# Performance work log

Hardware: AMD Instinct MI355X
Metric: run time of the kernel (lower is better)

## Reference

```python
import jax, jax.numpy as jnp
import numpy as np

N_EVENTS = 50000
TS_SIZE = 512
N_NEURONS = 256
LAMBDA_HOMEO = 0.25


def setup_inputs() -> dict:
    key = jax.random.key(0)
    k1, k2 = jax.random.split(key)
    # event time surfaces (nonnegative, like torch surfaces)
    all_ts = jax.random.uniform(k1, (N_EVENTS, TS_SIZE), dtype=jnp.float32)
    # synapses.weight ~ U[0,1), as in torch.nn.init.uniform_(a=0,b=1)
    W = jax.random.uniform(k2, (N_NEURONS, TS_SIZE), dtype=jnp.float32)
    cumhisto = jnp.ones((N_NEURONS,), dtype=jnp.float32)
    return {"all_ts": all_ts, "W": W, "cumhisto": cumhisto}


def reference(all_ts, W, cumhisto):
    """Training branch (learning_flag=True, homeo_flag=True) of hotslayer.forward.

    Sequential per-event: normalize ts, cosine-like scores beta, homeostatic gain
    picks the winner, winner row of W is pulled toward ts, histogram incremented.
    Returns (per-event winners [N_EVENTS], final W [N,TS], final cumhisto [N]).
    """
    n_neurons = W.shape[0]

    def step(carry, ts):
        W, ch = carry
        ts = ts / jnp.linalg.norm(ts)
        w_norm = jnp.linalg.norm(W, axis=1)          # [N]
        beta = (W @ ts) / w_norm                      # [N]
        gain = jnp.exp(LAMBDA_HOMEO * (1.0 - n_neurons * ch / ch.sum()))
        n_star = jnp.argmax(gain * beta)
        Ck = W[n_star]                                # [TS]
        alpha = 0.01 / (1.0 + ch[n_star] / 20000.0)
        W = W.at[n_star].set(Ck + alpha * beta[n_star] * (ts - Ck))
        ch = ch.at[n_star].add(1.0)
        return (W, ch), n_star

    (W_f, ch_f), winners = jax.lax.scan(step, (W, cumhisto), all_ts)
    return winners, W_f, ch_f
```

## Files before the change

### kernel.cpp

```cpp
#include <hip/hip_runtime.h>
#include <hip/hip_bf16.h>

#define N_EVENTS 50000
#define TS 512
#define NN 256
#define BATCH 512
#define SUB 64
#define LAMB 0.25f
#define NB 98

#define RLF(v, l) __int_as_float(__builtin_amdgcn_readlane(__float_as_int(v), (l)))
#define RLI(v, l) __builtin_amdgcn_readlane((v), (l))
#define FRCP(x) __builtin_amdgcn_rcpf(x)
#define FRSQ(x) __builtin_amdgcn_rsqf(x)
#define DPP_MAXF(x, ctrl)                                                            \
    { int _s = __builtin_amdgcn_update_dpp(__float_as_int(x), __float_as_int(x),     \
                                           (ctrl), 0xF, 0xF, false);                 \
      (x) = fmaxf((x), __int_as_float(_s)); }


__global__ __launch_bounds__(256)
void inv_kernel(const float* __restrict__ ts, float* __restrict__ inv)
{
    __shared__ double red[256];
    const int e = blockIdx.x;
    const int d = threadIdx.x;
    const float* row = ts + (size_t)e * TS;
    float x0 = row[d], x1 = row[d + 256];
    red[d] = (double)x0 * x0 + (double)x1 * x1;
    __syncthreads();
    for (int st = 128; st > 0; st >>= 1) {
        if (d < st) red[d] += red[d + st];
        __syncthreads();
    }
    if (d == 0) inv[e] = (float)(1.0 / sqrt(red[0]));
}

__global__ __launch_bounds__(256)
void init_kernel(const float* __restrict__ chin, float* __restrict__ ch,
                 float* Pn0, float* Pn1, float* phi0, float* phi1,
                 float* c0, float* c1, float* d0, float* d1,
                 int* w0, int* w1)
{
    int i = blockIdx.x * 256 + threadIdx.x;
    if (i < NN) { ch[i] = chin[i]; Pn0[i] = 1.f; Pn1[i] = 1.f; }
    if (i < BATCH) {
        phi0[i] = 0.f; phi1[i] = 0.f; c0[i] = 0.f; c1[i] = 0.f;
        d0[i] = 0.f; d1[i] = 0.f; w0[i] = 0; w1[i] = 0;
    }
}


__device__ void gram_tile(float* SH, const float* __restrict__ ts,
                          const float* __restrict__ inv,
                          int astart, int as, int bstart2, int bs2,
                          int be, int bf, float* __restrict__ outp, int transpose)
{
    float* At = SH;
    float* Bt = SH + 64 * 33;
    if (be * 64 >= as || bf * 64 >= bs2) return;
    const int tx = threadIdx.x & 15, ty = threadIdx.x >> 4;
    float acc[4][4] = {};
    for (int kt = 0; kt < TS; kt += 32) {
        for (int it = threadIdx.x; it < 64 * 32; it += 256) {
            int r = it >> 5, c = it & 31;
            int ra = be * 64 + r, rb = bf * 64 + r;
            At[r * 33 + c] = (ra < as) ? ts[(size_t)(astart + ra) * TS + kt + c] : 0.f;
            Bt[r * 33 + c] = (rb < bs2) ? ts[(size_t)(bstart2 + rb) * TS + kt + c] : 0.f;
        }
        __syncthreads();
#pragma unroll
        for (int kk = 0; kk < 32; ++kk) {
            float av[4], bv[4];
#pragma unroll
            for (int i = 0; i < 4; ++i) av[i] = At[(ty * 4 + i) * 33 + kk];
#pragma unroll
            for (int j = 0; j < 4; ++j) bv[j] = Bt[(tx * 4 + j) * 33 + kk];
#pragma unroll
            for (int i = 0; i < 4; ++i)
#pragma unroll
                for (int j = 0; j < 4; ++j)
                    acc[i][j] += av[i] * bv[j];
        }
        __syncthreads();
    }
#pragma unroll
    for (int i = 0; i < 4; ++i) {
        int e = be * 64 + ty * 4 + i;
        if (e >= as) continue;
        float ie = inv[astart + e];
#pragma unroll
        for (int j = 0; j < 4; ++j) {
            int f = bf * 64 + tx * 4 + j;
            if (f >= bs2) continue;
            float v = acc[i][j] * ie * inv[bstart2 + f];
            if (transpose) outp[(size_t)f * BATCH + e] = v;
            else           outp[(size_t)e * BATCH + f] = v;
        }
    }
}

__global__ __launch_bounds__(256)
void gram_kernel(const float* __restrict__ ts, const float* __restrict__ inv,
                 float* __restrict__ outp, int astart, int as, int bstart2, int bs2,
                 int upper, int transpose)
{
    __shared__ float SHg[64 * 33 * 2];
    if (upper && (int)blockIdx.y < (int)blockIdx.x) return;
    gram_tile(SHg, ts, inv, astart, as, bstart2, bs2, blockIdx.x, blockIdx.y,
              outp, transpose);
}


__device__ void neuron_body(float* shf, double* red,
    const float* __restrict__ ts, const float* __restrict__ inv,
    const float* __restrict__ Wsrc, float* __restrict__ wdst,
    const int* __restrict__ winPrev, const float* __restrict__ phiPrev,
    const float* __restrict__ PnPrev,
    float* __restrict__ wn2W, float* __restrict__ S2W,
    const float* __restrict__ chbuf, float* __restrict__ chout,
    int n, int bprev_start, int bs_prev, int bnext_start, int bs_next)
{
    int* winS = (int*)shf;
    float* phiS = shf + 512;
    float* WL = shf + 1024;
    const int d = threadIdx.x;
    for (int i = d; i < bs_prev; i += 256) { winS[i] = winPrev[i]; phiS[i] = phiPrev[i]; }
    __syncthreads();
    const float Pf = PnPrev[n];
    float w0 = Wsrc[n * TS + d];
    float w1 = Wsrc[n * TS + d + 256];
    double a0 = 0.0, a1 = 0.0;
    for (int e = 0; e < bs_prev; ++e) {
        if (winS[e] == n) {
            double coef = (double)phiS[e];
            float iv = inv[bprev_start + e];
            const float* tr = ts + (size_t)(bprev_start + e) * TS;
            a0 += coef * (double)(tr[d] * iv);
            a1 += coef * (double)(tr[d + 256] * iv);
        }
    }
    w0 = (float)((double)Pf * ((double)w0 + a0));
    w1 = (float)((double)Pf * ((double)w1 + a1));
    wdst[n * TS + d] = w0;
    wdst[n * TS + d + 256] = w1;
    WL[d] = w0; WL[d + 256] = w1;
    if (wn2W) {
        red[d] = (double)w0 * w0 + (double)w1 * w1;
        __syncthreads();
        for (int st = 128; st > 0; st >>= 1) {
            if (d < st) red[d] += red[d + st];
            __syncthreads();
        }
        if (d == 0) wn2W[n] = (float)red[0];
    } else {
        __syncthreads();
    }
    if (bs_next > 0) {
#pragma unroll
        for (int rep = 0; rep < 2; ++rep) {
            int f = d + rep * 256;
            if (f < bs_next) {
                double acc = 0.0;
                const float* tr = ts + (size_t)(bnext_start + f) * TS;
                for (int k = 0; k < TS; ++k) acc += (double)tr[k] * (double)WL[k];
                S2W[f * NN + n] = (float)(acc * (double)inv[bnext_start + f]);
            }
        }
    }
    if (chout && d == 0) chout[n] = chbuf[n];
}

__global__ __launch_bounds__(256)
void neuron_kernel(const float* __restrict__ ts, const float* __restrict__ inv,
    const float* __restrict__ Wsrc, float* __restrict__ wdst,
    const int* __restrict__ winPrev, const float* __restrict__ phiPrev,
    const float* __restrict__ PnPrev,
    float* __restrict__ wn2W, float* __restrict__ S2W,
    const float* __restrict__ chbuf, float* __restrict__ chout,
    int bprev_start, int bs_prev, int bnext_start, int bs_next)
{
    __shared__ float SHN[1536];
    __shared__ double redN[256];
    neuron_body(SHN, redN, ts, inv, Wsrc, wdst, winPrev, phiPrev, PnPrev,
                wn2W, S2W, chbuf, chout, blockIdx.x,
                bprev_start, bs_prev, bnext_start, bs_next);
}


__global__ __launch_bounds__(256)
void fix_kernel(const float* __restrict__ S2r, const float* __restrict__ GxTr,
    const int* __restrict__ winPrev, const float* __restrict__ phiPrev,
    const float* __restrict__ cPrev, const float* __restrict__ dPrev,
    const float* __restrict__ PnPrev, const float* __restrict__ wn2b,
    float* __restrict__ S0corr, float* __restrict__ wn2start,
    int bs, int b0flag)
{
    __shared__ int winS[512];
    __shared__ float phiP[512];
    __shared__ float gr[512];
    __shared__ float cS[512];
    __shared__ float dS[512];
    const int tid = threadIdx.x;
    const int f = blockIdx.x;
    for (int i = tid; i < 512; i += 256) {
        int w = winPrev[i];
        winS[i] = w;
        phiP[i] = b0flag ? 0.f : phiPrev[i] * PnPrev[w];
        cS[i] = cPrev[i];
        dS[i] = dPrev[i];
        gr[i] = (b0flag || f >= bs) ? 0.f : GxTr[(size_t)f * BATCH + i];
    }
    __syncthreads();
    if (f < bs) {
        int n = tid;
        float acc = PnPrev[n] * S2r[f * NN + n];
        if (!b0flag) {
            for (int e = 0; e < 512; ++e)
                if (winS[e] == n) acc += phiP[e] * gr[e];
        }
        S0corr[f * NN + n] = acc;
    }
    if (f == 0 && tid < 64) {
        const int lane = tid;
        float w2[4];
#pragma unroll
        for (int k = 0; k < 4; ++k) w2[k] = wn2b[k * 64 + lane];
        for (int e = 0; e < 512; ++e) {
            float c = cS[e];
            if (c != 0.f) {
                int w = winS[e];
                int owner = w & 63, kk = w >> 6;
                float omc = 1.f - c;
                float t2 = 2.f * c * omc * dS[e] + c * c;
#pragma unroll
                for (int k = 0; k < 4; ++k)
                    if (lane == owner && k == kk) w2[k] = omc * omc * w2[k] + t2;
            }
        }
#pragma unroll
        for (int k = 0; k < 4; ++k) wn2start[k * 64 + lane] = w2[k];
    }
}


__device__ void block0_body(float* SH,
    const float* __restrict__ S0corr, const float* __restrict__ GwR,
    const float* __restrict__ wn2start, float* __restrict__ chbuf,
    int* __restrict__ winCur, float* __restrict__ phiCur,
    float* __restrict__ cCur, float* __restrict__ dotCur, float* __restrict__ PnCur,
    float* __restrict__ winners_out, int bstart, int bs)
{
    float* ACC = SH;
    float* GS  = SH + 16384;
    float* GL  = SH + 20480;
    int*   winL = (int*)(SH + 24576);
    float* phiL = SH + 25088;
    float* cL   = SH + 25600;
    float* dL   = SH + 26112;
    unsigned long long* CANDu = (unsigned long long*)(SH + 26624);
    float* SUMS = SH + 26640;

    const int tid = threadIdx.x, wid = tid >> 6, lane = tid & 63;
    const int widu = __builtin_amdgcn_readfirstlane(wid);
    const int myn = (wid << 6) + lane;

    const float KC = -(LAMB * 256.0f * 1.44269504f);
    float ch = chbuf[myn];
    float wn2v = wn2start[myn];
    float rn = FRSQ(wn2v);
    float al = 0.01f * FRCP(1.0f + ch * (1.0f / 20000.0f));
    float Pn = 1.0f;

    {
        float loc = ch;
#pragma unroll
        for (int off = 32; off > 0; off >>= 1) loc += __shfl_xor(loc, off, 64);
        if (lane == 0) SUMS[wid] = loc;
    }
    __syncthreads();
    const float Sbase = SUMS[0] + SUMS[1] + SUMS[2] + SUMS[3];

    const int nsub = (bs + SUB - 1) >> 6;
    for (int sub = 0; sub < nsub; ++sub) {
        const int s0 = sub << 6;
        const int cnt = min(SUB, bs - s0);
        __syncthreads();
        {
            const int n = tid;
            for (int f = 0; f < cnt; f += 8) {
                const float* src = S0corr + (size_t)(s0 + f) * NN + n;
                float v0 = src[0 * NN], v1 = src[1 * NN], v2 = src[2 * NN], v3 = src[3 * NN];
                float v4 = src[4 * NN], v5 = src[5 * NN], v6 = src[6 * NN], v7 = src[7 * NN];
                ACC[(f + 0) * NN + ((n + f + 0) & 255)] = v0;
                ACC[(f + 1) * NN + ((n + f + 1) & 255)] = v1;
                ACC[(f + 2) * NN + ((n + f + 2) & 255)] = v2;
                ACC[(f + 3) * NN + ((n + f + 3) & 255)] = v3;
                ACC[(f + 4) * NN + ((n + f + 4) & 255)] = v4;
                ACC[(f + 5) * NN + ((n + f + 5) & 255)] = v5;
                ACC[(f + 6) * NN + ((n + f + 6) & 255)] = v6;
                ACC[(f + 7) * NN + ((n + f + 7) & 255)] = v7;
            }
        }
        for (int it = tid; it < SUB * SUB; it += 256) {
            int t = it >> 6, f = it & 63;
            GS[it] = (t < cnt && f < cnt) ? GwR[(size_t)(s0 + t) * BATCH + s0 + f] : 0.f;
        }
        for (int base = 0; base < s0; base += 64) {
            {
                const int i0 = tid, i1 = tid + 256, i2 = tid + 512, i3 = tid + 768;
                for (int rep = 0; rep < 4096; rep += 1024) {
                    float g0 = GwR[(size_t)(base + ((i0 + rep) >> 6)) * BATCH + s0 + (i0 & 63)];
                    float g1 = GwR[(size_t)(base + ((i1 + rep) >> 6)) * BATCH + s0 + (i1 & 63)];
                    float g2 = GwR[(size_t)(base + ((i2 + rep) >> 6)) * BATCH + s0 + (i2 & 63)];
                    float g3 = GwR[(size_t)(base + ((i3 + rep) >> 6)) * BATCH + s0 + (i3 & 63)];
                    GL[i0 + rep] = g0; GL[i1 + rep] = g1;
                    GL[i2 + rep] = g2; GL[i3 + rep] = g3;
                }
            }
            int wreg = winL[base + lane];
            float preg = phiL[base + lane];
            __syncthreads();
            for (int j = 0; j < 64; ++j) {
                int wj = RLI(wreg, j);
                if ((wj & 3) == wid) {
                    float pj = RLF(preg, j);
                    if (lane < cnt)
                        ACC[lane * NN + ((wj + lane) & 255)] += pj * GL[j * 64 + lane];
                }
            }
            __syncthreads();
        }
        __syncthreads();

        float acur = ACC[myn & 255];
        for (int t = 0; t < cnt; ++t) {
            const int ib = s0 + t;
            const float K2 = KC * FRCP(Sbase + (float)ib);
            const bool havenext = (t + 1 < cnt);
            float anext = 0.f;
            if (havenext) anext = ACC[(t + 1) * NN + ((myn + t + 1) & 255)];
            const int forig = t + 1 + lane;
            const float gval = GS[t * SUB + (forig & 63)];

            const float pa = Pn * acur;
            const float beta = pa * rn;
            const float key = beta * exp2f(K2 * ch);
            float kmax = key;
            DPP_MAXF(kmax, 0x111); DPP_MAXF(kmax, 0x112); DPP_MAXF(kmax, 0x114);
            DPP_MAXF(kmax, 0x118); DPP_MAXF(kmax, 0x142); DPP_MAXF(kmax, 0x143);
            const float smax = RLF(kmax, 63);
            unsigned long long mm = __ballot(key == smax);
            if (lane == 0) {
                int nl = (int)__builtin_ctzll(mm);
                CANDu[((t & 1) << 2) + wid] =
                    ((unsigned long long)__float_as_uint(smax) << 32)
                    | (unsigned)(255 - ((wid << 6) + nl));
            }
            __syncthreads();
            const unsigned long long* cb = CANDu + ((t & 1) << 2);
            unsigned long long b0 = cb[0], b1 = cb[1], b2 = cb[2], b3 = cb[3];
            unsigned long long ba = b0 > b1 ? b0 : b1;
            unsigned long long bb = b2 > b3 ? b2 : b3;
            unsigned long long best = ba > bb ? ba : bb;
            int ns = 255 - (int)(best & 0xFFull);
            ns = __builtin_amdgcn_readfirstlane(ns);
            const int ksq = ns >> 6, owner = ns & 63;

            if (widu == ksq) {
                const float betas  = RLF(beta, owner);
                const float dots   = RLF(pa, owner);
                const float pold   = RLF(Pn, owner);
                const float alphas = RLF(al, owner);
                const float c    = alphas * betas;
                const float omc  = 1.0f - c;
                const float pnew = pold * omc;
                const float phi  = c * FRCP(pnew);
                const float g1   = RLF(gval, 0);
                if (lane == owner) {
                    wn2v = omc * omc * wn2v + 2.f * c * omc * dots + c * c;
                    rn = FRSQ(wn2v);
                    ch += 1.0f;
                    al = 0.01f * FRCP(1.0f + ch * (1.0f / 20000.0f));
                    Pn = pnew;
                    if (havenext) anext += phi * g1;
                }
                if (lane > 0 && forig < cnt)
                    ACC[forig * NN + ((ns + forig) & 255)] += phi * gval;
                if (lane == 0) {
                    winL[ib] = ns; phiL[ib] = phi;
                    cL[ib] = c; dL[ib] = dots;
                }
            }
            acur = anext;
        }
    }
    __syncthreads();
    chbuf[myn] = ch;
    PnCur[myn] = Pn;
    for (int i = tid; i < bs; i += 256) {
        int w = winL[i];
        winCur[i] = w;
        phiCur[i] = phiL[i];
        cCur[i] = cL[i];
        dotCur[i] = dL[i];
        winners_out[bstart + i] = (float)w;
    }
}


__global__ __launch_bounds__(256)
void fusedA_kernel(const float* __restrict__ ts, const float* __restrict__ inv,
    const float* __restrict__ S0corr, const float* __restrict__ GwR,
    float* __restrict__ GwW, float* __restrict__ GxTW,
    const float* __restrict__ wn2start, float* __restrict__ chbuf,
    const int* __restrict__ winPrev, const float* __restrict__ phiPrev,
    const float* __restrict__ PnPrev,
    int* __restrict__ winCur, float* __restrict__ phiCur,
    float* __restrict__ cCur, float* __restrict__ dotCur, float* __restrict__ PnCur,
    float* __restrict__ Wcur, float* __restrict__ wn2W, float* __restrict__ S2W,
    float* __restrict__ out, int b, int bstart, int bs, int bnext_start, int bs_next)
{
    __shared__ float SH[26656];
    const int bx = blockIdx.x;
    if (bx == 0) {
        block0_body(SH, S0corr, GwR, wn2start, chbuf,
                    winCur, phiCur, cCur, dotCur, PnCur, out, bstart, bs);
    } else if (bx <= NN) {
        neuron_body(SH, (double*)(SH + 1536), ts, inv, Wcur, Wcur,
                    winPrev, phiPrev, PnPrev, wn2W, S2W, nullptr, nullptr,
                    bx - 1, bstart - BATCH, (b == 0) ? 0 : BATCH,
                    bnext_start, bs_next);
    } else {
        int job = bx - (NN + 1);
        if (bs_next <= 0) return;
        if (job < 64) {
            gram_tile(SH, ts, inv, bstart, bs, bnext_start, bs_next,
                      job >> 3, job & 7, GxTW, 1);
        } else {
            int jw = job - 64;
            int be = 0;
            while (jw >= 8 - be) { jw -= 8 - be; ++be; }
            int bf = be + jw;
            gram_tile(SH, ts, inv, bnext_start, bs_next, bnext_start, bs_next,
                      be, bf, GwW, 0);
        }
    }
}


__global__ __launch_bounds__(256)
void winit_kernel(const float* __restrict__ Wcur, const float* __restrict__ chin,
                  float* __restrict__ ch, float* __restrict__ wn2, float* __restrict__ rn)
{
    __shared__ double red[256];
    const int n = blockIdx.x;
    const int d = threadIdx.x;
    float w0 = Wcur[n * TS + d], w1 = Wcur[n * TS + d + 256];
    red[d] = (double)w0 * w0 + (double)w1 * w1;
    __syncthreads();
    for (int st = 128; st > 0; st >>= 1) {
        if (d < st) red[d] += red[d + st];
        __syncthreads();
    }
    if (d == 0) {
        double s = red[0];
        wn2[n] = (float)s;
        rn[n]  = (float)(1.0 / sqrt(s));
        ch[n]  = chin[n];
    }
}

__global__ __launch_bounds__(256)
void s0_gemm_kernel(const float* __restrict__ ts, const float* __restrict__ Wcur,
                    const float* __restrict__ inv, float* __restrict__ S0P,
                    int bstart, int bs)
{
    __shared__ float At[64][33];
    __shared__ float Bt[64][33];
    const int bf = blockIdx.x;
    const int bn = blockIdx.y;
    if (bf * 64 >= bs) return;
    const int tx = threadIdx.x & 15, ty = threadIdx.x >> 4;
    double acc[4][4] = {};
    for (int kt = 0; kt < TS; kt += 32) {
        for (int it = threadIdx.x; it < 64 * 32; it += 256) {
            int r = it >> 5, c = it & 31;
            int row = bf * 64 + r;
            At[r][c] = (row < bs) ? ts[(size_t)(bstart + row) * TS + kt + c] : 0.f;
            Bt[r][c] = Wcur[(bn * 64 + r) * TS + kt + c];
        }
        __syncthreads();
#pragma unroll
        for (int kk = 0; kk < 32; ++kk) {
            float av[4], bv[4];
#pragma unroll
            for (int i = 0; i < 4; ++i) av[i] = At[ty * 4 + i][kk];
#pragma unroll
            for (int j = 0; j < 4; ++j) bv[j] = Bt[tx * 4 + j][kk];
#pragma unroll
            for (int i = 0; i < 4; ++i)
#pragma unroll
                for (int j = 0; j < 4; ++j)
                    acc[i][j] += (double)av[i] * (double)bv[j];
        }
        __syncthreads();
    }
#pragma unroll
    for (int i = 0; i < 4; ++i) {
        int f = bf * 64 + ty * 4 + i;
        if (f >= bs) continue;
        double iv = (double)inv[bstart + f];
#pragma unroll
        for (int j = 0; j < 4; ++j) {
            int n = bn * 64 + tx * 4 + j;
            S0P[f * NN + n] = (float)(acc[i][j] * iv);
        }
    }
}

__global__ __launch_bounds__(256)
void seq_step_kernel(const float* __restrict__ S0P, const float* __restrict__ Gb,
                     float* __restrict__ ch_g, const float* __restrict__ wn2_g,
                     const float* __restrict__ rn_g, float* __restrict__ Pn_g,
                     float* __restrict__ phi_g, int* __restrict__ win_g,
                     float* __restrict__ winners_out, int bstart, int bs)
{
    __shared__ float ACC[SUB * NN];
    __shared__ float GS[SUB * SUB];
    __shared__ float GL[SUB * SUB];
    __shared__ int   winL[BATCH];
    __shared__ float phiL[BATCH];

    const int tid = threadIdx.x;
    const int wid = tid >> 6;
    const int lane = tid & 63;

    float ch[4] = {0, 0, 0, 0}, wn2v[4] = {1, 1, 1, 1};
    float rn[4] = {1, 1, 1, 1}, Pn[4] = {1, 1, 1, 1};
    float Ssum = 1.f, sinv = 1.f;
    if (wid == 0) {
#pragma unroll
        for (int k = 0; k < 4; ++k) {
            int n = k * 64 + lane;
            ch[k]   = ch_g[n];
            wn2v[k] = wn2_g[n];
            rn[k]   = rn_g[n];
            Pn[k]   = 1.0f;
        }
        float loc = ch[0] + ch[1] + ch[2] + ch[3];
#pragma unroll
        for (int off = 32; off > 0; off >>= 1) loc += __shfl_xor(loc, off, 64);
        Ssum = loc;
        sinv = 1.0f / Ssum;
    }

    const int nsub = (bs + SUB - 1) >> 6;
    for (int sub = 0; sub < nsub; ++sub) {
        const int s0 = sub << 6;
        const int cnt = min(SUB, bs - s0);
        __syncthreads();

        for (int it = tid; it < cnt * NN; it += 256) {
            int r = it >> 8, n = it & 255;
            ACC[r * NN + ((n + r) & 255)] = S0P[(s0 + r) * NN + n];
        }
        for (int it = tid; it < cnt * SUB; it += 256) {
            int t = it >> 6, f = it & 63;
            GS[t * SUB + f] = (f < cnt) ? Gb[(s0 + t) * BATCH + s0 + f] : 0.f;
        }
        __syncthreads();

        for (int base = 0; base < s0; base += 64) {
            for (int it = tid; it < 64 * 64; it += 256)
                GL[it] = Gb[(base + (it >> 6)) * BATCH + s0 + (it & 63)];
            int   wreg = winL[base + lane];
            float preg = phiL[base + lane];
            __syncthreads();
            for (int j = 0; j < 64; ++j) {
                int wj = RLI(wreg, j);
                if ((wj & 3) == wid) {
                    float pj = RLF(preg, j);
                    if (lane < cnt)
                        ACC[lane * NN + ((wj + lane) & 255)] += pj * GL[j * 64 + lane];
                }
            }
            __syncthreads();
        }

        if (wid == 0) {
            float acur[4];
#pragma unroll
            for (int k = 0; k < 4; ++k) acur[k] = ACC[(k * 64 + lane) & 255];

            for (int t = 0; t < cnt; ++t) {
                const bool havenext = (t + 1 < cnt);
                float anext[4] = {0.f, 0.f, 0.f, 0.f};
                if (havenext) {
                    const int r = t + 1;
#pragma unroll
                    for (int k = 0; k < 4; ++k)
                        anext[k] = ACC[r * NN + ((k * 64 + lane + r) & 255)];
                }
                const int forig = t + 1 + lane;
                const float gval = GS[t * SUB + (forig & 63)];

                const float gmul = 256.0f * sinv;
                float beta[4], key[4];
                float kmax;
#pragma unroll
                for (int k = 0; k < 4; ++k) {
                    float dot = Pn[k] * acur[k];
                    beta[k] = dot * rn[k];
                    float frac = ch[k] * gmul;
                    float gain = __expf(LAMB * (1.0f - frac));
                    key[k] = gain * beta[k];
                }
                kmax = fmaxf(fmaxf(key[0], key[1]), fmaxf(key[2], key[3]));
                DPP_MAXF(kmax, 0x111); DPP_MAXF(kmax, 0x112); DPP_MAXF(kmax, 0x114);
                DPP_MAXF(kmax, 0x118); DPP_MAXF(kmax, 0x142); DPP_MAXF(kmax, 0x143);
                const float smax = RLF(kmax, 63);

                unsigned long long m0 = __ballot(key[0] == smax);
                unsigned long long m1 = __ballot(key[1] == smax);
                unsigned long long m2 = __ballot(key[2] == smax);
                unsigned long long m3 = __ballot(key[3] == smax);
                int ns = m0 ? (int)__builtin_ctzll(m0)
                       : m1 ? 64  + (int)__builtin_ctzll(m1)
                       : m2 ? 128 + (int)__builtin_ctzll(m2)
                            : 192 + (int)__builtin_ctzll(m3);
                ns = __builtin_amdgcn_readfirstlane(ns);
                const int owner = ns & 63, ks = ns >> 6;

                float bsel = (ks == 0) ? beta[0] : (ks == 1) ? beta[1] : (ks == 2) ? beta[2] : beta[3];
                float csel = (ks == 0) ? ch[0]   : (ks == 1) ? ch[1]   : (ks == 2) ? ch[2]   : ch[3];
                float asel = (ks == 0) ? acur[0] : (ks == 1) ? acur[1] : (ks == 2) ? acur[2] : acur[3];
                float psel = (ks == 0) ? Pn[0]   : (ks == 1) ? Pn[1]   : (ks == 2) ? Pn[2]   : Pn[3];
                const float betas = RLF(bsel, owner);
                const float chs   = RLF(csel, owner);
                const float dots  = RLF(psel * asel, owner);
                const float pold  = RLF(psel, owner);

                const float alpha = 0.01f / (1.0f + chs / 20000.0f);
                const float c    = alpha * betas;
                const float omc  = 1.0f - c;
                const float pnew = pold * omc;
                const float phi  = c / pnew;
                const float g1   = RLF(gval, 0);

#pragma unroll
                for (int k = 0; k < 4; ++k) {
                    bool me = (lane == owner) && (k == ks);
                    if (me) {
                        wn2v[k] = omc * omc * wn2v[k] + 2.f * c * omc * dots + c * c;
                        rn[k] = 1.0f / sqrtf(wn2v[k]);
                        ch[k] += 1.0f;
                        Pn[k] = pnew;
                        anext[k] += phi * g1;
                    }
                }
                if (lane > 0 && forig < cnt)
                    ACC[forig * NN + ((ns + forig) & 255)] += phi * gval;

                const int ib = s0 + t;
                if (lane == 0) {
                    winL[ib] = ns; phiL[ib] = phi;
                    win_g[ib] = ns; phi_g[ib] = phi;
                    winners_out[bstart + ib] = (float)ns;
                }
                Ssum += 1.0f;
                sinv = 1.0f / Ssum;
                if (havenext) {
#pragma unroll
                    for (int k = 0; k < 4; ++k) acur[k] = anext[k];
                }
            }
        }
        __syncthreads();
    }

    if (wid == 0) {
#pragma unroll
        for (int k = 0; k < 4; ++k) {
            int n = k * 64 + lane;
            ch_g[n] = ch[k];
            Pn_g[n] = Pn[k];
        }
    }
}

__global__ __launch_bounds__(256)
void wupdate_kernel(const float* __restrict__ ts, const float* __restrict__ inv,
                    const int* __restrict__ win_g, const float* __restrict__ phi_g,
                    const float* __restrict__ Pn_g, float* __restrict__ Wcur,
                    float* __restrict__ wn2_g, float* __restrict__ rn_g,
                    int bstart, int bs)
{
    __shared__ int   winS[BATCH];
    __shared__ float phiS[BATCH];
    __shared__ double red[256];
    const int n = blockIdx.x;
    const int d = threadIdx.x;
    for (int i = d; i < bs; i += 256) { winS[i] = win_g[i]; phiS[i] = phi_g[i]; }
    __syncthreads();
    const float Pf = Pn_g[n];
    float w0 = Wcur[n * TS + d];
    float w1 = Wcur[n * TS + d + 256];
    double a0 = 0.0, a1 = 0.0;
    for (int ib = 0; ib < bs; ++ib) {
        if (winS[ib] == n) {
            double coef = (double)phiS[ib] * (double)Pf;
            float iv = inv[bstart + ib];
            const float* tr = ts + (size_t)(bstart + ib) * TS;
            a0 += coef * (double)(tr[d] * iv);
            a1 += coef * (double)(tr[d + 256] * iv);
        }
    }
    w0 = (float)((double)Pf * (double)w0 + a0);
    w1 = (float)((double)Pf * (double)w1 + a1);
    Wcur[n * TS + d] = w0;
    Wcur[n * TS + d + 256] = w1;
    red[d] = (double)w0 * w0 + (double)w1 * w1;
    __syncthreads();
    for (int st = 128; st > 0; st >>= 1) {
        if (d < st) red[d] += red[d + st];
        __syncthreads();
    }
    if (d == 0) {
        double s = red[0];
        wn2_g[n] = (float)s;
        rn_g[n]  = (float)(1.0 / sqrt(s));
    }
}

__global__ __launch_bounds__(256)
void final_kernel(const float* __restrict__ Wcur, const float* __restrict__ ch,
                  float* __restrict__ out)
{
    int i = blockIdx.x * 256 + threadIdx.x;
    if (i < NN * TS) out[N_EVENTS + i] = Wcur[i];
    else if (i < NN * TS + NN) out[N_EVENTS + i] = ch[i - NN * TS];
}


extern "C" void kernel_launch(void* const* d_in, const int* in_sizes, int n_in,
                              void* d_out, int out_size, void* d_ws, size_t ws_size,
                              hipStream_t stream)
{
    const float* ts   = (const float*)d_in[0];
    const float* W0   = (const float*)d_in[1];
    const float* chin = (const float*)d_in[2];
    float* out = (float*)d_out;
    float* ws  = (float*)d_ws;

    const size_t FULL_FLOATS = 1628544;
    if (ws_size >= FULL_FLOATS * sizeof(float)) {
        float* inv  = ws + 0;
        float* Wcur = ws + 50048;
        float* ch   = ws + 181120;
        float* wn2b[2] = { ws + 181376, ws + 181632 };
        float* wn2s = ws + 181888;
        float* Pn[2]  = { ws + 182144, ws + 182400 };
        float* phi[2] = { ws + 182656, ws + 183168 };
        float* cE[2]  = { ws + 183680, ws + 184192 };
        float* dE[2]  = { ws + 184704, ws + 185216 };
        int*   win[2] = { (int*)(ws + 185728), (int*)(ws + 186240) };
        float* S2[2]  = { ws + 186752, ws + 317824 };
        float* S0c    = ws + 448896;
        float* GxT[2] = { ws + 579968, ws + 842112 };
        float* Gw[2]  = { ws + 1104256, ws + 1366400 };

        hipMemcpyAsync(Wcur, W0, (size_t)NN * TS * sizeof(float),
                       hipMemcpyDeviceToDevice, stream);
        inv_kernel<<<N_EVENTS, 256, 0, stream>>>(ts, inv);
        init_kernel<<<2, 256, 0, stream>>>(chin, ch, Pn[0], Pn[1], phi[0], phi[1],
                                           cE[0], cE[1], dE[0], dE[1], win[0], win[1]);
        neuron_kernel<<<NN, 256, 0, stream>>>(ts, inv, Wcur, Wcur,
            win[1], phi[1], Pn[1], wn2b[0], S2[0], nullptr, nullptr,
            0, 0, 0, BATCH);
        gram_kernel<<<dim3(8, 8), 256, 0, stream>>>(ts, inv, Gw[0],
            0, BATCH, 0, BATCH, 1, 0);

        for (int b = 0; b < NB; ++b) {
            const int cs = b & 1, ps = 1 - cs;
            const int bstart = b * BATCH;
            const int bs = min(BATCH, N_EVENTS - bstart);
            const int bnext = bstart + BATCH;
            const int bsn = (b == NB - 1) ? 0 : min(BATCH, N_EVENTS - bnext);

            fix_kernel<<<BATCH, 256, 0, stream>>>(S2[cs], GxT[cs],
                win[ps], phi[ps], cE[ps], dE[ps], Pn[ps], wn2b[cs],
                S0c, wn2s, bs, (b == 0) ? 1 : 0);

            const int grid = (b == NB - 1) ? (NN + 1) : (NN + 1 + 100);
            fusedA_kernel<<<grid, 256, 0, stream>>>(ts, inv, S0c, Gw[cs],
                Gw[ps], GxT[ps], wn2s, ch,
                win[ps], phi[ps], Pn[ps],
                win[cs], phi[cs], cE[cs], dE[cs], Pn[cs],
                Wcur, wn2b[ps], S2[ps],
                out, b, bstart, bs, bnext, bsn);
        }
        neuron_kernel<<<NN, 256, 0, stream>>>(ts, inv, Wcur, out + N_EVENTS,
            win[1], phi[1], Pn[1], nullptr, nullptr, ch, out + N_EVENTS + NN * TS,
            97 * BATCH, 336, 0, 0);
    } else {
        float* inv  = ws + 0;
        float* Wcur = ws + 50048;
        float* ch   = ws + 181120;
        float* wn2  = ws + 181376;
        float* rn   = ws + 181632;
        float* Pn   = ws + 181888;
        float* phi  = ws + 182144;
        int*   win  = (int*)(ws + 182656);
        float* S0P  = ws + 183168;
        float* G    = ws + 314240;

        hipMemcpyAsync(Wcur, W0, (size_t)NN * TS * sizeof(float),
                       hipMemcpyDeviceToDevice, stream);
        inv_kernel<<<N_EVENTS, 256, 0, stream>>>(ts, inv);
        winit_kernel<<<NN, 256, 0, stream>>>(Wcur, chin, ch, wn2, rn);

        for (int b = 0; b < NB; ++b) {
            int bstart = b * BATCH;
            int bs = min(BATCH, N_EVENTS - bstart);
            s0_gemm_kernel<<<dim3(8, 4), 256, 0, stream>>>(ts, Wcur, inv, S0P, bstart, bs);
            gram_kernel<<<dim3(8, 8), 256, 0, stream>>>(ts, inv, G,
                bstart, bs, bstart, bs, 1, 0);
            seq_step_kernel<<<1, 256, 0, stream>>>(S0P, G, ch, wn2, rn, Pn, phi, win,
                                                   out, bstart, bs);
            wupdate_kernel<<<NN, 256, 0, stream>>>(ts, inv, win, phi, Pn, Wcur,
                                                   wn2, rn, bstart, bs);
        }
        final_kernel<<<(NN * TS + NN + 255) / 256, 256, 0, stream>>>(Wcur, ch, out);
    }
}
```

Baseline: 56.76 ms.

## Run serial winner-selection loop in a single wave to drop per-event block barriers

Result: faster. 54.52 ms (-3.9%).

```diff
diff --git a/kernel.cpp b/kernel.cpp
--- a/kernel.cpp
+++ b/kernel.cpp
@@ -258,28 +258,26 @@
     float* phiL = SH + 25088;
     float* cL   = SH + 25600;
     float* dL   = SH + 26112;
-    unsigned long long* CANDu = (unsigned long long*)(SH + 26624);
-    float* SUMS = SH + 26640;
 
     const int tid = threadIdx.x, wid = tid >> 6, lane = tid & 63;
-    const int widu = __builtin_amdgcn_readfirstlane(wid);
-    const int myn = (wid << 6) + lane;
 
     const float KC = -(LAMB * 256.0f * 1.44269504f);
-    float ch = chbuf[myn];
-    float wn2v = wn2start[myn];
-    float rn = FRSQ(wn2v);
-    float al = 0.01f * FRCP(1.0f + ch * (1.0f / 20000.0f));
-    float Pn = 1.0f;
-
-    {
-        float loc = ch;
+    float ch0 = 0, ch1 = 0, ch2 = 0, ch3 = 0;
+    float w20 = 1, w21 = 1, w22 = 1, w23 = 1;
+    float rn0 = 1, rn1 = 1, rn2 = 1, rn3 = 1;
+    float Pn0 = 1, Pn1 = 1, Pn2 = 1, Pn3 = 1;
+    float Sbase = 1.f;
+    if (wid == 0) {
+        ch0 = chbuf[lane];        ch1 = chbuf[64 + lane];
+        ch2 = chbuf[128 + lane];  ch3 = chbuf[192 + lane];
+        w20 = wn2start[lane];       w21 = wn2start[64 + lane];
+        w22 = wn2start[128 + lane]; w23 = wn2start[192 + lane];
+        rn0 = FRSQ(w20); rn1 = FRSQ(w21); rn2 = FRSQ(w22); rn3 = FRSQ(w23);
+        float loc = ch0 + ch1 + ch2 + ch3;
 #pragma unroll
         for (int off = 32; off > 0; off >>= 1) loc += __shfl_xor(loc, off, 64);
-        if (lane == 0) SUMS[wid] = loc;
-    }
-    __syncthreads();
-    const float Sbase = SUMS[0] + SUMS[1] + SUMS[2] + SUMS[3];
+        Sbase = loc;
+    }
 
     const int nsub = (bs + SUB - 1) >> 6;
     for (int sub = 0; sub < nsub; ++sub) {
@@ -333,71 +331,102 @@
         }
         __syncthreads();
 
-        float acur = ACC[myn & 255];
-        for (int t = 0; t < cnt; ++t) {
-            const int ib = s0 + t;
-            const float K2 = KC * FRCP(Sbase + (float)ib);
-            const bool havenext = (t + 1 < cnt);
-            float anext = 0.f;
-            if (havenext) anext = ACC[(t + 1) * NN + ((myn + t + 1) & 255)];
-            const int forig = t + 1 + lane;
-            const float gval = GS[t * SUB + (forig & 63)];
-
-            const float pa = Pn * acur;
-            const float beta = pa * rn;
-            const float key = beta * exp2f(K2 * ch);
-            float kmax = key;
-            DPP_MAXF(kmax, 0x111); DPP_MAXF(kmax, 0x112); DPP_MAXF(kmax, 0x114);
-            DPP_MAXF(kmax, 0x118); DPP_MAXF(kmax, 0x142); DPP_MAXF(kmax, 0x143);
-            const float smax = RLF(kmax, 63);
-            unsigned long long mm = __ballot(key == smax);
-            if (lane == 0) {
-                int nl = (int)__builtin_ctzll(mm);
-                CANDu[((t & 1) << 2) + wid] =
-                    ((unsigned long long)__float_as_uint(smax) << 32)
-                    | (unsigned)(255 - ((wid << 6) + nl));
-            }
-            __syncthreads();
-            const unsigned long long* cb = CANDu + ((t & 1) << 2);
-            unsigned long long b0 = cb[0], b1 = cb[1], b2 = cb[2], b3 = cb[3];
-            unsigned long long ba = b0 > b1 ? b0 : b1;
-            unsigned long long bb = b2 > b3 ? b2 : b3;
-            unsigned long long best = ba > bb ? ba : bb;
-            int ns = 255 - (int)(best & 0xFFull);
-            ns = __builtin_amdgcn_readfirstlane(ns);
-            const int ksq = ns >> 6, owner = ns & 63;
-
-            if (widu == ksq) {
-                const float betas  = RLF(beta, owner);
-                const float dots   = RLF(pa, owner);
-                const float pold   = RLF(Pn, owner);
-                const float alphas = RLF(al, owner);
-                const float c    = alphas * betas;
-                const float omc  = 1.0f - c;
-                const float pnew = pold * omc;
-                const float phi  = c * FRCP(pnew);
-                const float g1   = RLF(gval, 0);
-                if (lane == owner) {
-                    wn2v = omc * omc * wn2v + 2.f * c * omc * dots + c * c;
-                    rn = FRSQ(wn2v);
-                    ch += 1.0f;
-                    al = 0.01f * FRCP(1.0f + ch * (1.0f / 20000.0f));
-                    Pn = pnew;
-                    if (havenext) anext += phi * g1;
-                }
-                if (lane > 0 && forig < cnt)
-                    ACC[forig * NN + ((ns + forig) & 255)] += phi * gval;
-                if (lane == 0) {
-                    winL[ib] = ns; phiL[ib] = phi;
-                    cL[ib] = c; dL[ib] = dots;
+        if (wid == 0) {
+            float a0 = ACC[(lane) & 255];
+            float a1 = ACC[(64 + lane) & 255];
+            float a2 = ACC[(128 + lane) & 255];
+            float a3 = ACC[(192 + lane) & 255];
+
+            for (int t0 = 0; t0 < cnt; t0 += 8) {
+#pragma unroll
+                for (int u = 0; u < 8; ++u) {
+                    const int t = t0 + u;
+                    const int ib = s0 + t;
+                    const float K2 = KC * FRCP(Sbase + (float)ib);
+                    const bool hn = (t + 1 < cnt);
+                    float n0 = 0.f, n1 = 0.f, n2 = 0.f, n3 = 0.f;
+                    if (hn) {
+                        const int r = t + 1;
+                        n0 = ACC[r * NN + ((lane + r) & 255)];
+                        n1 = ACC[r * NN + ((64 + lane + r) & 255)];
+                        n2 = ACC[r * NN + ((128 + lane + r) & 255)];
+                        n3 = ACC[r * NN + ((192 + lane + r) & 255)];
+                    }
+                    const int fo = t + 1 + lane;
+                    const float gval = GS[t * SUB + (fo & 63)];
+
+                    const float pa0 = Pn0 * a0, pa1 = Pn1 * a1;
+                    const float pa2 = Pn2 * a2, pa3 = Pn3 * a3;
+                    const float b0 = pa0 * rn0, b1 = pa1 * rn1;
+                    const float b2 = pa2 * rn2, b3 = pa3 * rn3;
+                    const float k0 = b0 * exp2f(K2 * ch0);
+                    const float k1 = b1 * exp2f(K2 * ch1);
+                    const float k2 = b2 * exp2f(K2 * ch2);
+                    const float k3 = b3 * exp2f(K2 * ch3);
+                    float km = fmaxf(fmaxf(k0, k1), fmaxf(k2, k3));
+                    DPP_MAXF(km, 0x111); DPP_MAXF(km, 0x112); DPP_MAXF(km, 0x114);
+                    DPP_MAXF(km, 0x118); DPP_MAXF(km, 0x142); DPP_MAXF(km, 0x143);
+                    const float smax = RLF(km, 63);
+
+                    unsigned long long m0 = __ballot(k0 == smax);
+                    unsigned long long m1 = __ballot(k1 == smax);
+                    unsigned long long m2 = __ballot(k2 == smax);
+                    unsigned long long m3 = __ballot(k3 == smax);
+                    int ns = m0 ? (int)__builtin_ctzll(m0)
+                           : m1 ? 64  + (int)__builtin_ctzll(m1)
+                           : m2 ? 128 + (int)__builtin_ctzll(m2)
+                                : 192 + (int)__builtin_ctzll(m3);
+                    ns = __builtin_amdgcn_readfirstlane(ns);
+                    const int owner = ns & 63, ks = ns >> 6;
+
+                    const float bsel  = (ks == 0) ? b0  : (ks == 1) ? b1  : (ks == 2) ? b2  : b3;
+                    const float pasel = (ks == 0) ? pa0 : (ks == 1) ? pa1 : (ks == 2) ? pa2 : pa3;
+                    const float Psel  = (ks == 0) ? Pn0 : (ks == 1) ? Pn1 : (ks == 2) ? Pn2 : Pn3;
+                    const float csel  = (ks == 0) ? ch0 : (ks == 1) ? ch1 : (ks == 2) ? ch2 : ch3;
+                    const float betas = RLF(bsel, owner);
+                    const float pas   = RLF(pasel, owner);
+                    const float pold  = RLF(Psel, owner);
+                    const float chs   = RLF(csel, owner);
+
+                    const bool dorm = (lane > 0) && (fo < cnt);
+                    int rix = 0; float rold = 0.f;
+                    if (dorm) { rix = fo * NN + ((ns + fo) & 255); rold = ACC[rix]; }
+
+                    const float alpha = 0.01f * FRCP(1.0f + chs * (1.0f / 20000.0f));
+                    const float c    = alpha * betas;
+                    const float omc  = 1.0f - c;
+                    const float pnew = pold * omc;
+                    const float phi  = c * FRCP(pnew);
+                    const float g1   = RLF(gval, 0);
+
+                    const bool lo = (lane == owner);
+                    if (lo && ks == 0) { w20 = omc * omc * w20 + 2.f * c * omc * pas + c * c;
+                        rn0 = FRSQ(w20); ch0 += 1.f; Pn0 = pnew; n0 += phi * g1; }
+                    if (lo && ks == 1) { w21 = omc * omc * w21 + 2.f * c * omc * pas + c * c;
+                        rn1 = FRSQ(w21); ch1 += 1.f; Pn1 = pnew; n1 += phi * g1; }
+                    if (lo && ks == 2) { w22 = omc * omc * w22 + 2.f * c * omc * pas + c * c;
+                        rn2 = FRSQ(w22); ch2 += 1.f; Pn2 = pnew; n2 += phi * g1; }
+                    if (lo && ks == 3) { w23 = omc * omc * w23 + 2.f * c * omc * pas + c * c;
+                        rn3 = FRSQ(w23); ch3 += 1.f; Pn3 = pnew; n3 += phi * g1; }
+
+                    if (lane == 0) {
+                        winL[ib] = ns; phiL[ib] = phi;
+                        cL[ib] = c; dL[ib] = pas;
+                    }
+                    if (dorm) ACC[rix] = rold + phi * gval;
+
+                    if (hn) { a0 = n0; a1 = n1; a2 = n2; a3 = n3; }
                 }
             }
-            acur = anext;
         }
     }
     __syncthreads();
-    chbuf[myn] = ch;
-    PnCur[myn] = Pn;
+    if (wid == 0) {
+        chbuf[lane] = ch0;        chbuf[64 + lane] = ch1;
+        chbuf[128 + lane] = ch2;  chbuf[192 + lane] = ch3;
+        PnCur[lane] = Pn0;        PnCur[64 + lane] = Pn1;
+        PnCur[128 + lane] = Pn2;  PnCur[192 + lane] = Pn3;
+    }
     for (int i = tid; i < bs; i += 256) {
         int w = winL[i];
         winCur[i] = w;
```
